# Kernel tuning notes

Hardware: AMD Instinct MI355X
Metric: run time of the kernel (lower is better)

## Reference

```python
import jax, jax.numpy as jnp
import numpy as np

N_NODES = 100000
N_EDGES = 1600000
D = 64  # edge feature dim == node hidden dim


def setup_inputs() -> dict:
    key = jax.random.key(0)
    k1, k2, k3, k4, k5, k6, k7 = jax.random.split(key, 7)
    edges = jax.random.normal(k1, (N_EDGES, D), dtype=jnp.float32)
    nodes = jax.random.normal(k2, (N_NODES, D), dtype=jnp.float32)
    receivers = jax.random.randint(k3, (N_EDGES,), 0, N_NODES, dtype=jnp.int32)
    s = 1.0 / np.sqrt(D)
    w_ih = jax.random.normal(k4, (3 * D, D), dtype=jnp.float32) * s
    w_hh = jax.random.normal(k5, (3 * D, D), dtype=jnp.float32) * s
    b_ih = jax.random.normal(k6, (3 * D,), dtype=jnp.float32) * s
    b_hh = jax.random.normal(k7, (3 * D,), dtype=jnp.float32) * s
    return {"edges": edges, "nodes": nodes, "receivers": receivers,
            "w_ih": w_ih, "w_hh": w_hh, "b_ih": b_ih, "b_hh": b_hh}


def reference(edges, nodes, receivers, w_ih, w_hh, b_ih, b_hh):
    # Scatter-aggregate edge features into receiver nodes: [N, D]
    aggr = jax.ops.segment_sum(edges, receivers, num_segments=nodes.shape[0])
    # GRU cell update (PyTorch/equinox gate order: reset, update, new)
    gi = aggr @ w_ih.T + b_ih      # [N, 3D]
    gh = nodes @ w_hh.T + b_hh     # [N, 3D]
    i_r, i_z, i_n = jnp.split(gi, 3, axis=-1)
    h_r, h_z, h_n = jnp.split(gh, 3, axis=-1)
    r = jax.nn.sigmoid(i_r + h_r)
    z = jax.nn.sigmoid(i_z + h_z)
    n = jnp.tanh(i_n + r * h_n)
    new_nodes = (1.0 - z) * n + z * nodes
    return new_nodes
```

## Files before the change

kernel.cpp:

```cpp
#include <hip/hip_runtime.h>
#include <math.h>

#define N_NODES_C 100000
#define N_EDGES_C 1600000
#define DIM 64
#define G3 192
#define SCAN_B 1024
#define N_SCAN_BLOCKS ((N_NODES_C + SCAN_B - 1) / SCAN_B)

typedef short bf16x8 __attribute__((ext_vector_type(8)));
typedef float f32x4 __attribute__((ext_vector_type(4)));

__global__ void hist_kernel(const int* __restrict__ receivers,
                            int* __restrict__ count,
                            int* __restrict__ rank) {
    int e = blockIdx.x * blockDim.x + threadIdx.x;
    if (e >= N_EDGES_C) return;
    int r = receivers[e];
    rank[e] = __hip_atomic_fetch_add(&count[r], 1,
                                     __ATOMIC_RELAXED, __HIP_MEMORY_SCOPE_AGENT);
}

__global__ void scan1_kernel(const int* __restrict__ count,
                             int* __restrict__ offsets,
                             int* __restrict__ bsums) {
    __shared__ int wsum[16];
    const int gid  = blockIdx.x * SCAN_B + threadIdx.x;
    const int lane = threadIdx.x & 63;
    const int wv   = threadIdx.x >> 6;
    int c = (gid < N_NODES_C) ? count[gid] : 0;
    int x = c;
    #pragma unroll
    for (int o = 1; o < 64; o <<= 1) {
        int v = __shfl_up(x, o);
        if (lane >= o) x += v;
    }
    if (lane == 63) wsum[wv] = x;
    __syncthreads();
    if (wv == 0) {
        int s = (lane < 16) ? wsum[lane] : 0;
        #pragma unroll
        for (int o = 1; o < 16; o <<= 1) {
            int v = __shfl_up(s, o);
            if (lane >= o) s += v;
        }
        if (lane < 16) wsum[lane] = s;
    }
    __syncthreads();
    int woff = (wv == 0) ? 0 : wsum[wv - 1];
    if (gid < N_NODES_C) offsets[gid] = woff + x - c;
    if (threadIdx.x == SCAN_B - 1) bsums[blockIdx.x] = wsum[15];
}

__global__ void scan2_kernel(int* __restrict__ bsums) {
    __shared__ int w0tot;
    const int i    = threadIdx.x;
    const int lane = threadIdx.x & 63;
    const int wv   = threadIdx.x >> 6;
    int c = (i < N_SCAN_BLOCKS) ? bsums[i] : 0;
    int x = c;
    #pragma unroll
    for (int o = 1; o < 64; o <<= 1) {
        int v = __shfl_up(x, o);
        if (lane >= o) x += v;
    }
    if (wv == 0 && lane == 63) w0tot = x;
    __syncthreads();
    int add = (wv == 1) ? w0tot : 0;
    if (i < N_SCAN_BLOCKS) bsums[i] = add + x - c;
}

__global__ void permw_kernel(const int* __restrict__ receivers,
                             const int* __restrict__ offsets,
                             const int* __restrict__ bsums,
                             const int* __restrict__ rank,
                             int* __restrict__ perm) {
    int e = blockIdx.x * blockDim.x + threadIdx.x;
    if (e >= N_EDGES_C) return;
    int r = receivers[e];
    perm[offsets[r] + bsums[r >> 10] + rank[e]] = e;
}

__global__ __launch_bounds__(256)
void gather_kernel(const float* __restrict__ edges,
                   const int* __restrict__ perm,
                   const int* __restrict__ offsets,
                   const int* __restrict__ bsums,
                   const int* __restrict__ count,
                   float* __restrict__ aggr) {
    const int w    = (blockIdx.x << 2) | (threadIdx.x >> 6);
    const int lane = threadIdx.x & 63;
    if (w >= N_NODES_C) return;
    const int g    = lane >> 4;
    const int c4   = (lane & 15) << 2;
    const int start = offsets[w] + bsums[w >> 10];
    const int cnt   = count[w];

    float4 a0 = make_float4(0.f, 0.f, 0.f, 0.f);
    float4 a1 = a0, a2 = a0, a3 = a0;

    int done = 0;
    while (done < cnt) {
        const int pv  = perm[start + min(done + lane, cnt - 1)];
        const int lim = min(cnt - done, 64);
        const int nq  = (lim + 15) >> 4;
        for (int q = 0; q < nq; ++q) {
            const int rbase = q << 4;
            #pragma unroll
            for (int b = 0; b < 4; ++b) {
                const int rr  = rbase + (b << 2) + g;
                const int src = min(rr, lim - 1);
                const int e   = __shfl(pv, src);
                const float4 v = *reinterpret_cast<const float4*>(
                    edges + (size_t)e * DIM + c4);
                const float m = (rr < lim) ? 1.f : 0.f;
                if (b == 0) { a0.x += v.x*m; a0.y += v.y*m; a0.z += v.z*m; a0.w += v.w*m; }
                if (b == 1) { a1.x += v.x*m; a1.y += v.y*m; a1.z += v.z*m; a1.w += v.w*m; }
                if (b == 2) { a2.x += v.x*m; a2.y += v.y*m; a2.z += v.z*m; a2.w += v.w*m; }
                if (b == 3) { a3.x += v.x*m; a3.y += v.y*m; a3.z += v.z*m; a3.w += v.w*m; }
            }
        }
        done += 64;
    }

    float4 s;
    s.x = (a0.x + a1.x) + (a2.x + a3.x);
    s.y = (a0.y + a1.y) + (a2.y + a3.y);
    s.z = (a0.z + a1.z) + (a2.z + a3.z);
    s.w = (a0.w + a1.w) + (a2.w + a3.w);
    #pragma unroll
    for (int m = 16; m <= 32; m <<= 1) {
        s.x += __shfl_xor(s.x, m);
        s.y += __shfl_xor(s.y, m);
        s.z += __shfl_xor(s.z, m);
        s.w += __shfl_xor(s.w, m);
    }
    if (lane < 16) {
        *reinterpret_cast<float4*>(aggr + (size_t)w * DIM + c4) = s;
    }
}

__device__ __forceinline__ unsigned short bf16_rne(float f) {
    unsigned int u = __float_as_uint(f);
    return (unsigned short)((u + 0x7FFFu + ((u >> 16) & 1u)) >> 16);
}

__device__ __forceinline__ void stage_w(const float* __restrict__ w,
                                        unsigned short* whi,
                                        unsigned short* wlo, int tid) {
    #pragma unroll
    for (int i = 0; i < 6; ++i) {
        const int ci  = tid + i * 256;
        const int col = ci >> 3;
        const int ch  = ci & 7;
        const float4 f0 = *reinterpret_cast<const float4*>(w + col * 64 + ch * 8);
        const float4 f1 = *reinterpret_cast<const float4*>(w + col * 64 + ch * 8 + 4);
        const float f[8] = {f0.x, f0.y, f0.z, f0.w, f1.x, f1.y, f1.z, f1.w};
        unsigned int hi[4], lo[4];
        #pragma unroll
        for (int j = 0; j < 4; ++j) {
            const unsigned int u0 = __float_as_uint(f[2 * j]);
            const unsigned int u1 = __float_as_uint(f[2 * j + 1]);
            const float l0 = f[2 * j]     - __uint_as_float(u0 & 0xFFFF0000u);
            const float l1 = f[2 * j + 1] - __uint_as_float(u1 & 0xFFFF0000u);
            hi[j] = (u0 >> 16) | ((u1 >> 16) << 16);
            lo[j] = (unsigned int)bf16_rne(l0) | ((unsigned int)bf16_rne(l1) << 16);
        }
        const int addr = col * 64 + ((ch ^ (col & 7)) << 3);
        *reinterpret_cast<uint4*>(whi + addr) = make_uint4(hi[0], hi[1], hi[2], hi[3]);
        *reinterpret_cast<uint4*>(wlo + addr) = make_uint4(lo[0], lo[1], lo[2], lo[3]);
    }
}

__device__ __forceinline__ void stage_rows(const float* __restrict__ src,
                                           float* rows, int nb, int tid) {
    #pragma unroll
    for (int i = 0; i < 4; ++i) {
        const int idx = tid + i * 256;
        const int r = idx >> 4, c = idx & 15;
        float4 v = make_float4(0.f, 0.f, 0.f, 0.f);
        if (nb + r < N_NODES_C)
            v = *reinterpret_cast<const float4*>(src + (size_t)(nb + r) * 64 + (c << 2));
        *reinterpret_cast<float4*>(rows + r * 64 + ((c ^ (r & 15)) << 2)) = v;
    }
}

__global__ __launch_bounds__(256, 2)
void gru_mfma_kernel(float* aggr_out,
                     const float* __restrict__ nodes,
                     const float* __restrict__ w_ih,
                     const float* __restrict__ w_hh,
                     const float* __restrict__ b_ih,
                     const float* __restrict__ b_hh) {
    __shared__ __align__(16) unsigned short s_w[2 * 12288];
    __shared__ __align__(16) float s_rows[64 * 64];

    const int tid  = threadIdx.x;
    const int lane = tid & 63;
    const int wave = tid >> 6;
    const int nb   = blockIdx.x * 64;
    const int l15  = lane & 15;
    const int lg   = lane >> 4;

    float bir[4], biz[4], bin_[4], bhr[4], bhz[4], bhn[4];
    #pragma unroll
    for (int t = 0; t < 4; ++t) {
        const int o = l15 + (t << 4);
        bir[t] = b_ih[o]; biz[t] = b_ih[64 + o]; bin_[t] = b_ih[128 + o];
        bhr[t] = b_hh[o]; bhz[t] = b_hh[64 + o]; bhn[t] = b_hh[128 + o];
    }

    f32x4 accA[12], accB[12];
    #pragma unroll
    for (int ct = 0; ct < 12; ++ct) { accA[ct] = (f32x4)(0.f); accB[ct] = (f32x4)(0.f); }

    unsigned short* whi = s_w;
    unsigned short* wlo = s_w + 12288;
    const int arow = (wave << 4) + l15;

    stage_w(w_ih, whi, wlo, tid);
    stage_rows(aggr_out, s_rows, nb, tid);
    __syncthreads();

    #pragma unroll
    for (int kt = 0; kt < 2; ++kt) {
        const int c0 = kt * 8 + (lg << 1);
        const float4 fa = *reinterpret_cast<const float4*>(
            &s_rows[arow * 64 + ((c0 ^ l15) << 2)]);
        const float4 fb = *reinterpret_cast<const float4*>(
            &s_rows[arow * 64 + (((c0 + 1) ^ l15) << 2)]);
        const float f[8] = {fa.x, fa.y, fa.z, fa.w, fb.x, fb.y, fb.z, fb.w};
        union { bf16x8 v; unsigned int u[4]; } ahi, alo;
        #pragma unroll
        for (int j = 0; j < 4; ++j) {
            const unsigned int u0 = __float_as_uint(f[2 * j]);
            const unsigned int u1 = __float_as_uint(f[2 * j + 1]);
            const float l0 = f[2 * j]     - __uint_as_float(u0 & 0xFFFF0000u);
            const float l1 = f[2 * j + 1] - __uint_as_float(u1 & 0xFFFF0000u);
            ahi.u[j] = (u0 >> 16) | ((u1 >> 16) << 16);
            alo.u[j] = (unsigned int)bf16_rne(l0) | ((unsigned int)bf16_rne(l1) << 16);
        }
        #pragma unroll
        for (int ct = 0; ct < 12; ++ct) {
            const int col = ct * 16 + l15;
            const int sw  = (kt * 4 + lg) ^ (col & 7);
            const bf16x8 bhi = *reinterpret_cast<const bf16x8*>(&whi[col * 64 + (sw << 3)]);
            const bf16x8 blo = *reinterpret_cast<const bf16x8*>(&wlo[col * 64 + (sw << 3)]);
            accA[ct] = __builtin_amdgcn_mfma_f32_16x16x32_bf16(ahi.v, bhi, accA[ct], 0, 0, 0);
            accA[ct] = __builtin_amdgcn_mfma_f32_16x16x32_bf16(alo.v, bhi, accA[ct], 0, 0, 0);
            accA[ct] = __builtin_amdgcn_mfma_f32_16x16x32_bf16(ahi.v, blo, accA[ct], 0, 0, 0);
        }
    }
    __syncthreads();

    stage_w(w_hh, whi, wlo, tid);
    stage_rows(nodes, s_rows, nb, tid);
    __syncthreads();

    #pragma unroll
    for (int kt = 0; kt < 2; ++kt) {
        const int c0 = kt * 8 + (lg << 1);
        const float4 fa = *reinterpret_cast<const float4*>(
            &s_rows[arow * 64 + ((c0 ^ l15) << 2)]);
        const float4 fb = *reinterpret_cast<const float4*>(
            &s_rows[arow * 64 + (((c0 + 1) ^ l15) << 2)]);
        const float f[8] = {fa.x, fa.y, fa.z, fa.w, fb.x, fb.y, fb.z, fb.w};
        union { bf16x8 v; unsigned int u[4]; } ahi, alo;
        #pragma unroll
        for (int j = 0; j < 4; ++j) {
            const unsigned int u0 = __float_as_uint(f[2 * j]);
            const unsigned int u1 = __float_as_uint(f[2 * j + 1]);
            const float l0 = f[2 * j]     - __uint_as_float(u0 & 0xFFFF0000u);
            const float l1 = f[2 * j + 1] - __uint_as_float(u1 & 0xFFFF0000u);
            ahi.u[j] = (u0 >> 16) | ((u1 >> 16) << 16);
            alo.u[j] = (unsigned int)bf16_rne(l0) | ((unsigned int)bf16_rne(l1) << 16);
        }
        #pragma unroll
        for (int ct = 0; ct < 12; ++ct) {
            const int col = ct * 16 + l15;
            const int sw  = (kt * 4 + lg) ^ (col & 7);
            const bf16x8 bhi = *reinterpret_cast<const bf16x8*>(&whi[col * 64 + (sw << 3)]);
            const bf16x8 blo = *reinterpret_cast<const bf16x8*>(&wlo[col * 64 + (sw << 3)]);
            accB[ct] = __builtin_amdgcn_mfma_f32_16x16x32_bf16(ahi.v, bhi, accB[ct], 0, 0, 0);
            accB[ct] = __builtin_amdgcn_mfma_f32_16x16x32_bf16(alo.v, bhi, accB[ct], 0, 0, 0);
            accB[ct] = __builtin_amdgcn_mfma_f32_16x16x32_bf16(ahi.v, blo, accB[ct], 0, 0, 0);
        }
    }

    #pragma unroll
    for (int t = 0; t < 4; ++t) {
        #pragma unroll
        for (int rg = 0; rg < 4; ++rg) {
            const int rr   = (wave << 4) + (lg << 2) + rg;
            const int node = nb + rr;
            const int o    = l15 + (t << 4);
            const float ir = accA[t][rg]     + bir[t];
            const float iz = accA[4 + t][rg] + biz[t];
            const float inn= accA[8 + t][rg] + bin_[t];
            const float hr = accB[t][rg]     + bhr[t];
            const float hz = accB[4 + t][rg] + bhz[t];
            const float hn = accB[8 + t][rg] + bhn[t];
            const float r = 1.f / (1.f + __expf(-(ir + hr)));
            const float z = 1.f / (1.f + __expf(-(iz + hz)));
            float tt = inn + r * hn;
            tt = fminf(fmaxf(tt, -15.f), 15.f);
            const float e2 = __expf(2.f * tt);
            const float ng = (e2 - 1.f) / (e2 + 1.f);
            const int c = o >> 2;
            const float h = s_rows[rr * 64 + ((c ^ (rr & 15)) << 2) + (o & 3)];
            if (node < N_NODES_C)
                aggr_out[(size_t)node * 64 + o] = (1.f - z) * ng + z * h;
        }
    }
}

extern "C" void kernel_launch(void* const* d_in, const int* in_sizes, int n_in,
                              void* d_out, int out_size, void* d_ws, size_t ws_size,
                              hipStream_t stream) {
    const float* edges     = (const float*)d_in[0];
    const float* nodes     = (const float*)d_in[1];
    const int*   receivers = (const int*)d_in[2];
    const float* w_ih      = (const float*)d_in[3];
    const float* w_hh      = (const float*)d_in[4];
    const float* b_ih      = (const float*)d_in[5];
    const float* b_hh      = (const float*)d_in[6];
    float* out = (float*)d_out;

    int* ws      = (int*)d_ws;
    int* count   = ws;
    int* offsets = ws + N_NODES_C;
    int* rank    = ws + 2 * N_NODES_C;
    int* perm    = rank + N_EDGES_C;
    int* bsums   = perm + N_EDGES_C;

    hipMemsetAsync(count, 0, N_NODES_C * sizeof(int), stream);

    hist_kernel<<<(N_EDGES_C + 255) / 256, 256, 0, stream>>>(receivers, count, rank);
    scan1_kernel<<<N_SCAN_BLOCKS, SCAN_B, 0, stream>>>(count, offsets, bsums);
    scan2_kernel<<<1, 128, 0, stream>>>(bsums);
    permw_kernel<<<(N_EDGES_C + 255) / 256, 256, 0, stream>>>(receivers, offsets, bsums, rank, perm);

    gather_kernel<<<(N_NODES_C + 3) / 4, 256, 0, stream>>>(edges, perm, offsets, bsums, count, out);
    gru_mfma_kernel<<<(N_NODES_C + 63) / 64, 256, 0, stream>>>(out, nodes, w_ih, w_hh, b_ih, b_hh);
}
```

Measured before the change: 245.2 us.

## Pre-split weights, nodes and aggregates into swizzled bf16 hi/lo global images

Two new kernels convert the GRU weights and node features into pre-swizzled bf16 hi/lo images in workspace. The gather kernel now writes the aggregated rows directly in the same split layout. The GRU kernel then just copies these images into shared memory with vector loads, instead of converting fp32 to hi/lo in every block. This removes the per-block conversion arithmetic and the repeated weight conversion, at the cost of an extra full read/write pass over the node tensor and two more launches. The skip connection now uses hi+lo reconstructed nodes, a slight precision change.

Result: no change. 249.4 us (+1.7%).

```diff
diff --git a/kernel.cpp b/kernel.cpp
--- a/kernel.cpp
+++ b/kernel.cpp
@@ -10,6 +10,25 @@
 
 typedef short bf16x8 __attribute__((ext_vector_type(8)));
 typedef float f32x4 __attribute__((ext_vector_type(4)));
+
+__device__ __forceinline__ unsigned short bf16_rne(float f) {
+    unsigned int u = __float_as_uint(f);
+    return (unsigned short)((u + 0x7FFFu + ((u >> 16) & 1u)) >> 16);
+}
+
+__device__ __forceinline__ void split2(float f0, float f1,
+                                       unsigned int& hi, unsigned int& lo) {
+    const unsigned int u0 = __float_as_uint(f0);
+    const unsigned int u1 = __float_as_uint(f1);
+    const float l0 = f0 - __uint_as_float(u0 & 0xFFFF0000u);
+    const float l1 = f1 - __uint_as_float(u1 & 0xFFFF0000u);
+    hi = (u0 >> 16) | ((u1 >> 16) << 16);
+    lo = (unsigned int)bf16_rne(l0) | ((unsigned int)bf16_rne(l1) << 16);
+}
+
+__device__ __forceinline__ float bf16f(unsigned short h) {
+    return __uint_as_float(((unsigned int)h) << 16);
+}
 
 __global__ void hist_kernel(const int* __restrict__ receivers,
                             int* __restrict__ count,
@@ -81,13 +100,52 @@
     perm[offsets[r] + bsums[r >> 10] + rank[e]] = e;
 }
 
+__global__ void prep_w_kernel(const float* __restrict__ w_ih,
+                              const float* __restrict__ w_hh,
+                              unsigned short* __restrict__ img_w) {
+    const int ci  = blockIdx.x * 256 + threadIdx.x;
+    if (ci >= 3072) return;
+    const int mat = ci / 1536;
+    const int rem = ci - mat * 1536;
+    const int col = rem >> 3;
+    const int ch  = rem & 7;
+    const float* w = mat ? w_hh : w_ih;
+    const float4 f0 = *reinterpret_cast<const float4*>(w + col * 64 + ch * 8);
+    const float4 f1 = *reinterpret_cast<const float4*>(w + col * 64 + ch * 8 + 4);
+    unsigned int hi[4], lo[4];
+    split2(f0.x, f0.y, hi[0], lo[0]);
+    split2(f0.z, f0.w, hi[1], lo[1]);
+    split2(f1.x, f1.y, hi[2], lo[2]);
+    split2(f1.z, f1.w, hi[3], lo[3]);
+    unsigned short* dst = img_w + mat * 24576 + col * 64 + ((ch ^ (col & 7)) << 3);
+    *reinterpret_cast<uint4*>(dst)         = make_uint4(hi[0], hi[1], hi[2], hi[3]);
+    *reinterpret_cast<uint4*>(dst + 12288) = make_uint4(lo[0], lo[1], lo[2], lo[3]);
+}
+
+__global__ void prep_nodes_kernel(const float* __restrict__ nodes,
+                                  unsigned short* __restrict__ n_hi,
+                                  unsigned short* __restrict__ n_lo) {
+    const int t = blockIdx.x * 256 + threadIdx.x;
+    if (t >= N_NODES_C * 16) return;
+    const int row = t >> 4;
+    const int cc  = t & 15;
+    const float4 f = *reinterpret_cast<const float4*>(nodes + (size_t)row * 64 + cc * 4);
+    unsigned int h0, l0, h1, l1;
+    split2(f.x, f.y, h0, l0);
+    split2(f.z, f.w, h1, l1);
+    const int addr = row * 64 + (((cc >> 1) ^ (row & 7)) << 3) + ((cc & 1) << 2);
+    *reinterpret_cast<uint2*>(n_hi + addr) = make_uint2(h0, h1);
+    *reinterpret_cast<uint2*>(n_lo + addr) = make_uint2(l0, l1);
+}
+
 __global__ __launch_bounds__(256)
 void gather_kernel(const float* __restrict__ edges,
                    const int* __restrict__ perm,
                    const int* __restrict__ offsets,
                    const int* __restrict__ bsums,
                    const int* __restrict__ count,
-                   float* __restrict__ aggr) {
+                   unsigned short* __restrict__ a_hi,
+                   unsigned short* __restrict__ a_lo) {
     const int w    = (blockIdx.x << 2) | (threadIdx.x >> 6);
     const int lane = threadIdx.x & 63;
     if (w >= N_NODES_C) return;
@@ -136,64 +194,27 @@
         s.w += __shfl_xor(s.w, m);
     }
     if (lane < 16) {
-        *reinterpret_cast<float4*>(aggr + (size_t)w * DIM + c4) = s;
-    }
-}
-
-__device__ __forceinline__ unsigned short bf16_rne(float f) {
-    unsigned int u = __float_as_uint(f);
-    return (unsigned short)((u + 0x7FFFu + ((u >> 16) & 1u)) >> 16);
-}
-
-__device__ __forceinline__ void stage_w(const float* __restrict__ w,
-                                        unsigned short* whi,
-                                        unsigned short* wlo, int tid) {
-    #pragma unroll
-    for (int i = 0; i < 6; ++i) {
-        const int ci  = tid + i * 256;
-        const int col = ci >> 3;
-        const int ch  = ci & 7;
-        const float4 f0 = *reinterpret_cast<const float4*>(w + col * 64 + ch * 8);
-        const float4 f1 = *reinterpret_cast<const float4*>(w + col * 64 + ch * 8 + 4);
-        const float f[8] = {f0.x, f0.y, f0.z, f0.w, f1.x, f1.y, f1.z, f1.w};
-        unsigned int hi[4], lo[4];
-        #pragma unroll
-        for (int j = 0; j < 4; ++j) {
-            const unsigned int u0 = __float_as_uint(f[2 * j]);
-            const unsigned int u1 = __float_as_uint(f[2 * j + 1]);
-            const float l0 = f[2 * j]     - __uint_as_float(u0 & 0xFFFF0000u);
-            const float l1 = f[2 * j + 1] - __uint_as_float(u1 & 0xFFFF0000u);
-            hi[j] = (u0 >> 16) | ((u1 >> 16) << 16);
-            lo[j] = (unsigned int)bf16_rne(l0) | ((unsigned int)bf16_rne(l1) << 16);
-        }
-        const int addr = col * 64 + ((ch ^ (col & 7)) << 3);
-        *reinterpret_cast<uint4*>(whi + addr) = make_uint4(hi[0], hi[1], hi[2], hi[3]);
-        *reinterpret_cast<uint4*>(wlo + addr) = make_uint4(lo[0], lo[1], lo[2], lo[3]);
-    }
-}
-
-__device__ __forceinline__ void stage_rows(const float* __restrict__ src,
-                                           float* rows, int nb, int tid) {
-    #pragma unroll
-    for (int i = 0; i < 4; ++i) {
-        const int idx = tid + i * 256;
-        const int r = idx >> 4, c = idx & 15;
-        float4 v = make_float4(0.f, 0.f, 0.f, 0.f);
-        if (nb + r < N_NODES_C)
-            v = *reinterpret_cast<const float4*>(src + (size_t)(nb + r) * 64 + (c << 2));
-        *reinterpret_cast<float4*>(rows + r * 64 + ((c ^ (r & 15)) << 2)) = v;
+        const int l15 = lane;
+        unsigned int h0, l0, h1, l1;
+        split2(s.x, s.y, h0, l0);
+        split2(s.z, s.w, h1, l1);
+        const int addr = w * 64 + ((((l15) >> 1) ^ (w & 7)) << 3) + ((l15 & 1) << 2);
+        *reinterpret_cast<uint2*>(a_hi + addr) = make_uint2(h0, h1);
+        *reinterpret_cast<uint2*>(a_lo + addr) = make_uint2(l0, l1);
     }
 }
 
 __global__ __launch_bounds__(256, 2)
-void gru_mfma_kernel(float* aggr_out,
-                     const float* __restrict__ nodes,
-                     const float* __restrict__ w_ih,
-                     const float* __restrict__ w_hh,
+void gru_mfma_kernel(const unsigned short* __restrict__ img_w,
+                     const unsigned short* __restrict__ aggr_hi,
+                     const unsigned short* __restrict__ aggr_lo,
+                     const unsigned short* __restrict__ nodes_hi,
+                     const unsigned short* __restrict__ nodes_lo,
                      const float* __restrict__ b_ih,
-                     const float* __restrict__ b_hh) {
-    __shared__ __align__(16) unsigned short s_w[2 * 12288];
-    __shared__ __align__(16) float s_rows[64 * 64];
+                     const float* __restrict__ b_hh,
+                     float* __restrict__ out) {
+    __shared__ __align__(16) unsigned short s_w[24576];
+    __shared__ __align__(16) unsigned short s_a[8192];
 
     const int tid  = threadIdx.x;
     const int lane = tid & 63;
@@ -201,6 +222,7 @@
     const int nb   = blockIdx.x * 64;
     const int l15  = lane & 15;
     const int lg   = lane >> 4;
+    const int arow = (wave << 4) + l15;
 
     float bir[4], biz[4], bin_[4], bhr[4], bhz[4], bhn[4];
     #pragma unroll
@@ -214,76 +236,70 @@
     #pragma unroll
     for (int ct = 0; ct < 12; ++ct) { accA[ct] = (f32x4)(0.f); accB[ct] = (f32x4)(0.f); }
 
-    unsigned short* whi = s_w;
-    unsigned short* wlo = s_w + 12288;
-    const int arow = (wave << 4) + l15;
-
-    stage_w(w_ih, whi, wlo, tid);
-    stage_rows(aggr_out, s_rows, nb, tid);
+    {
+        const uint4* wsrc = reinterpret_cast<const uint4*>(img_w);
+        uint4* wdst = reinterpret_cast<uint4*>(s_w);
+        #pragma unroll
+        for (int i = 0; i < 12; ++i) wdst[tid + i * 256] = wsrc[tid + i * 256];
+        const uint4* hsrc = reinterpret_cast<const uint4*>(aggr_hi + (size_t)nb * 64);
+        const uint4* lsrc = reinterpret_cast<const uint4*>(aggr_lo + (size_t)nb * 64);
+        uint4* adst = reinterpret_cast<uint4*>(s_a);
+        #pragma unroll
+        for (int i = 0; i < 2; ++i) {
+            adst[tid + i * 256]       = hsrc[tid + i * 256];
+            adst[512 + tid + i * 256] = lsrc[tid + i * 256];
+        }
+    }
     __syncthreads();
 
     #pragma unroll
     for (int kt = 0; kt < 2; ++kt) {
-        const int c0 = kt * 8 + (lg << 1);
-        const float4 fa = *reinterpret_cast<const float4*>(
-            &s_rows[arow * 64 + ((c0 ^ l15) << 2)]);
-        const float4 fb = *reinterpret_cast<const float4*>(
-            &s_rows[arow * 64 + (((c0 + 1) ^ l15) << 2)]);
-        const float f[8] = {fa.x, fa.y, fa.z, fa.w, fb.x, fb.y, fb.z, fb.w};
-        union { bf16x8 v; unsigned int u[4]; } ahi, alo;
-        #pragma unroll
-        for (int j = 0; j < 4; ++j) {
-            const unsigned int u0 = __float_as_uint(f[2 * j]);
-            const unsigned int u1 = __float_as_uint(f[2 * j + 1]);
-            const float l0 = f[2 * j]     - __uint_as_float(u0 & 0xFFFF0000u);
-            const float l1 = f[2 * j + 1] - __uint_as_float(u1 & 0xFFFF0000u);
-            ahi.u[j] = (u0 >> 16) | ((u1 >> 16) << 16);
-            alo.u[j] = (unsigned int)bf16_rne(l0) | ((unsigned int)bf16_rne(l1) << 16);
-        }
+        const int ach = ((kt * 4 + lg) ^ (arow & 7)) << 3;
+        const bf16x8 ahi = *reinterpret_cast<const bf16x8*>(&s_a[arow * 64 + ach]);
+        const bf16x8 alo = *reinterpret_cast<const bf16x8*>(&s_a[4096 + arow * 64 + ach]);
         #pragma unroll
         for (int ct = 0; ct < 12; ++ct) {
             const int col = ct * 16 + l15;
-            const int sw  = (kt * 4 + lg) ^ (col & 7);
-            const bf16x8 bhi = *reinterpret_cast<const bf16x8*>(&whi[col * 64 + (sw << 3)]);
-            const bf16x8 blo = *reinterpret_cast<const bf16x8*>(&wlo[col * 64 + (sw << 3)]);
-            accA[ct] = __builtin_amdgcn_mfma_f32_16x16x32_bf16(ahi.v, bhi, accA[ct], 0, 0, 0);
-            accA[ct] = __builtin_amdgcn_mfma_f32_16x16x32_bf16(alo.v, bhi, accA[ct], 0, 0, 0);
-            accA[ct] = __builtin_amdgcn_mfma_f32_16x16x32_bf16(ahi.v, blo, accA[ct], 0, 0, 0);
-        }
-    }
-    __syncthreads();
-
-    stage_w(w_hh, whi, wlo, tid);
-    stage_rows(nodes, s_rows, nb, tid);
+            const int sw  = ((kt * 4 + lg) ^ (col & 7)) << 3;
+            const bf16x8 bhi = *reinterpret_cast<const bf16x8*>(&s_w[col * 64 + sw]);
+            const bf16x8 blo = *reinterpret_cast<const bf16x8*>(&s_w[12288 + col * 64 + sw]);
+            accA[ct] = __builtin_amdgcn_mfma_f32_16x16x32_bf16(ahi, bhi, accA[ct], 0, 0, 0);
+            accA[ct] = __builtin_amdgcn_mfma_f32_16x16x32_bf16(alo, bhi, accA[ct], 0, 0, 0);
+            accA[ct] = __builtin_amdgcn_mfma_f32_16x16x32_bf16(ahi, blo, accA[ct], 0, 0, 0);
+        }
+    }
+    __syncthreads();
+
+    {
+        const uint4* wsrc = reinterpret_cast<const uint4*>(img_w + 24576);
+        uint4* wdst = reinterpret_cast<uint4*>(s_w);
+        #pragma unroll
+        for (int i = 0; i < 12; ++i) wdst[tid + i * 256] = wsrc[tid + i * 256];
+        const uint4* hsrc = reinterpret_cast<const uint4*>(nodes_hi + (size_t)nb * 64);
+        const uint4* lsrc = reinterpret_cast<const uint4*>(nodes_lo + (size_t)nb * 64);
+        uint4* adst = reinterpret_cast<uint4*>(s_a);
+        #pragma unroll
+        for (int i = 0; i < 2; ++i) {
+            adst[tid + i * 256]       = hsrc[tid + i * 256];
+            adst[512 + tid + i * 256] = lsrc[tid + i * 256];
+        }
+    }
     __syncthreads();
 
     #pragma unroll
     for (int kt = 0; kt < 2; ++kt) {
-        const int c0 = kt * 8 + (lg << 1);
-        const float4 fa = *reinterpret_cast<const float4*>(
-            &s_rows[arow * 64 + ((c0 ^ l15) << 2)]);
-        const float4 fb = *reinterpret_cast<const float4*>(
-            &s_rows[arow * 64 + (((c0 + 1) ^ l15) << 2)]);
-        const float f[8] = {fa.x, fa.y, fa.z, fa.w, fb.x, fb.y, fb.z, fb.w};
-        union { bf16x8 v; unsigned int u[4]; } ahi, alo;
-        #pragma unroll
-        for (int j = 0; j < 4; ++j) {
-            const unsigned int u0 = __float_as_uint(f[2 * j]);
-            const unsigned int u1 = __float_as_uint(f[2 * j + 1]);
-            const float l0 = f[2 * j]     - __uint_as_float(u0 & 0xFFFF0000u);
-            const float l1 = f[2 * j + 1] - __uint_as_float(u1 & 0xFFFF0000u);
-            ahi.u[j] = (u0 >> 16) | ((u1 >> 16) << 16);
-            alo.u[j] = (unsigned int)bf16_rne(l0) | ((unsigned int)bf16_rne(l1) << 16);
-        }
+        const int ach = ((kt * 4 + lg) ^ (arow & 7)) << 3;
+        const bf16x8 ahi = *reinterpret_cast<const bf16x8*>(&s_a[arow * 64 + ach]);
+        const bf16x8 alo = *reinterpret_cast<const bf16x8*>(&s_a[4096 + arow * 64 + ach]);
         #pragma unroll
         for (int ct = 0; ct < 12; ++ct) {
             const int col = ct * 16 + l15;
-            const int sw  = (kt * 4 + lg) ^ (col & 7);
-            const bf16x8 bhi = *reinterpret_cast<const bf16x8*>(&whi[col * 64 + (sw << 3)]);
-            const bf16x8 blo = *reinterpret_cast<const bf16x8*>(&wlo[col * 64 + (sw << 3)]);
-            accB[ct] = __builtin_amdgcn_mfma_f32_16x16x32_bf16(ahi.v, bhi, accB[ct], 0, 0, 0);
-            accB[ct] = __builtin_amdgcn_mfma_f32_16x16x32_bf16(alo.v, bhi, accB[ct], 0, 0, 0);
-            accB[ct] = __builtin_amdgcn_mfma_f32_16x16x32_bf16(ahi.v, blo, accB[ct], 0, 0, 0);
+            const int sw  = ((kt * 4 + lg) ^ (col & 7)) << 3;
+            const bf16x8 bhi = *reinterpret_cast<const bf16x8*>(&s_w[col * 64 + sw]);
+            const bf16x8 blo = *reinterpret_cast<const bf16x8*>(&s_w[12288 + col * 64 + sw]);
+            accB[ct] = __builtin_amdgcn_mfma_f32_16x16x32_bf16(ahi, bhi, accB[ct], 0, 0, 0);
+            accB[ct] = __builtin_amdgcn_mfma_f32_16x16x32_bf16(alo, bhi, accB[ct], 0, 0, 0);
+            accB[ct] = __builtin_amdgcn_mfma_f32_16x16x32_bf16(ahi, blo, accB[ct], 0, 0, 0);
         }
     }
 
@@ -306,10 +322,10 @@
             tt = fminf(fmaxf(tt, -15.f), 15.f);
             const float e2 = __expf(2.f * tt);
             const float ng = (e2 - 1.f) / (e2 + 1.f);
-            const int c = o >> 2;
-            const float h = s_rows[rr * 64 + ((c ^ (rr & 15)) << 2) + (o & 3)];
+            const int idx = rr * 64 + (((o >> 3) ^ (rr & 7)) << 3) + (o & 7);
+            const float h = bf16f(s_a[idx]) + bf16f(s_a[4096 + idx]);
             if (node < N_NODES_C)
-                aggr_out[(size_t)node * 64 + o] = (1.f - z) * ng + z * h;
+                out[(size_t)node * 64 + o] = (1.f - z) * ng + z * h;
         }
     }
 }
@@ -332,14 +348,25 @@
     int* rank    = ws + 2 * N_NODES_C;
     int* perm    = rank + N_EDGES_C;
     int* bsums   = perm + N_EDGES_C;
+    unsigned short* img_w   = (unsigned short*)(ws + 3400192);
+    unsigned short* aggr_hi = img_w + 4 * 12288;
+    unsigned short* aggr_lo = aggr_hi + (size_t)N_NODES_C * 64;
+    unsigned short* n_hi    = aggr_lo + (size_t)N_NODES_C * 64;
+    unsigned short* n_lo    = n_hi    + (size_t)N_NODES_C * 64;
 
     hipMemsetAsync(count, 0, N_NODES_C * sizeof(int), stream);
+
+    prep_w_kernel<<<12, 256, 0, stream>>>(w_ih, w_hh, img_w);
+    prep_nodes_kernel<<<(N_NODES_C * 16 + 255) / 256, 256, 0, stream>>>(nodes, n_hi, n_lo);
 
     hist_kernel<<<(N_EDGES_C + 255) / 256, 256, 0, stream>>>(receivers, count, rank);
     scan1_kernel<<<N_SCAN_BLOCKS, SCAN_B, 0, stream>>>(count, offsets, bsums);
     scan2_kernel<<<1, 128, 0, stream>>>(bsums);
     permw_kernel<<<(N_EDGES_C + 255) / 256, 256, 0, stream>>>(receivers, offsets, bsums, rank, perm);
 
-    gather_kernel<<<(N_NODES_C + 3) / 4, 256, 0, stream>>>(edges, perm, offsets, bsums, count, out);
-    gru_mfma_kernel<<<(N_NODES_C + 63) / 64, 256, 0, stream>>>(out, nodes, w_ih, w_hh, b_ih, b_hh);
-}
+    gather_kernel<<<(N_NODES_C + 3) / 4, 256, 0, stream>>>(
+        edges, perm, offsets, bsums, count, aggr_hi, aggr_lo);
+
+    gru_mfma_kernel<<<(N_NODES_C + 63) / 64, 256, 0, stream>>>(
+        img_w, aggr_hi, aggr_lo, n_hi, n_lo, b_ih, b_hh, out);
+}
```
